# Kernel optimization log

Hardware: AMD Instinct MI355X
Metric: run time of the kernel (lower is better)

Reference implementation:

```python
import jax, jax.numpy as jnp
import numpy as np

N_NODES = 50000
N_EDGES = 800000
ND = 64
ED = 32
MSG = 128
HID = 256
N_AGENTS = 25000


def setup_inputs() -> dict:
    key = jax.random.key(0)
    ks = jax.random.split(key, 12)
    s = lambda k, shape, fan: jax.random.normal(k, shape, jnp.float32) / np.sqrt(fan)
    return {
        'node_feats': jax.random.normal(ks[0], (N_NODES, ND), jnp.float32),
        'edge_feats': jax.random.normal(ks[1], (N_EDGES, ED), jnp.float32),
        'W_msg1': s(ks[2], (2 * ND + ED, HID), 2 * ND + ED),
        'b_msg1': jnp.zeros((HID,), jnp.float32),
        'W_msg2': s(ks[3], (HID, MSG), HID),
        'b_msg2': jnp.zeros((MSG,), jnp.float32),
        'w_gate': s(ks[4], (MSG, 1), MSG),
        'b_gate': jnp.zeros((1,), jnp.float32),
        'W_h1': s(ks[5], (MSG, HID), MSG),
        'b_h1': jnp.zeros((HID,), jnp.float32),
        'W_h2': s(ks[6], (HID, HID), HID),
        'b_h2': jnp.zeros((HID,), jnp.float32),
        'W_out': s(ks[7], (HID, 1), HID),
        'b_out': jnp.zeros((1,), jnp.float32),
        'senders': jax.random.randint(ks[8], (N_EDGES,), 0, N_NODES, jnp.int32),
        'receivers': jax.random.randint(ks[9], (N_EDGES,), 0, N_NODES, jnp.int32),
        'n_agents': N_AGENTS,
    }


def reference(node_feats, edge_feats, W_msg1, b_msg1, W_msg2, b_msg2,
              w_gate, b_gate, W_h1, b_h1, W_h2, b_h2, W_out, b_out,
              senders, receivers, n_agents):
    n_nodes = node_feats.shape[0]
    # gather sender/receiver features, build edge messages (gather-transform)
    msg_in = jnp.concatenate(
        [node_feats[senders], node_feats[receivers], edge_feats], axis=-1)  # [E, 2*ND+ED]
    h = jax.nn.relu(msg_in @ W_msg1 + b_msg1)                               # [E, HID]
    msg = jax.nn.relu(h @ W_msg2 + b_msg2)                                  # [E, MSG]
    # per-receiver segment softmax attention
    logits = (msg @ w_gate + b_gate)[:, 0]                                  # [E]
    seg_max = jax.ops.segment_max(logits, receivers, num_segments=n_nodes)  # [N]
    e = jnp.exp(logits - seg_max[receivers])                                # [E]
    denom = jax.ops.segment_sum(e, receivers, num_segments=n_nodes)         # [N]
    attn = e / (denom[receivers] + 1e-9)                                    # [E]
    # scatter-aggregate messages to nodes
    aggr = jax.ops.segment_sum(attn[:, None] * msg, receivers,
                               num_segments=n_nodes)                        # [N, MSG]
    # node_type == 0: agent nodes are the first n_agents nodes
    x = aggr[:n_agents]                                                     # [A, MSG]
    # head MLP
    x = jax.nn.relu(x @ W_h1 + b_h1)
    x = jax.nn.relu(x @ W_h2 + b_h2)
    # Dense(1) + tanh
    return jnp.tanh(x @ W_out + b_out)                                      # [A, 1]
```

## Files before the change

### kernel.cpp

```cpp
#include <hip/hip_runtime.h>
#include <hip/hip_bf16.h>

#define N_NODES  50000
#define N_EDGES  800000
#define ND       64
#define ED       32
#define MSGD     128
#define HIDD     256
#define N_AGENTS 25000
#define EPAD     800064

typedef _Float16 f16;
typedef __attribute__((ext_vector_type(4))) _Float16 f16x4;
typedef __attribute__((ext_vector_type(8))) _Float16 f16x8;
typedef __attribute__((ext_vector_type(4))) float f32x4;
typedef unsigned short u16;
typedef unsigned int   u32;
typedef unsigned long long u64;

__global__ __launch_bounds__(256) void pack_weights(
    const float* __restrict__ W1, const float* __restrict__ W2,
    const float* __restrict__ Wh1, const float* __restrict__ Wh2,
    f16* __restrict__ F1, f16* __restrict__ F2,
    f16* __restrict__ F3, f16* __restrict__ F4)
{
    int tid  = blockIdx.x * 256 + threadIdx.x;
    int grp  = tid >> 6, lane = tid & 63;
    const float* W; f16* D; int NT, stride, gl;
    if      (grp < 80)  { W = W1;  D = F1; NT = 16; stride = 256; gl = grp; }
    else if (grp < 144) { W = W2;  D = F2; NT = 8;  stride = 128; gl = grp - 80; }
    else if (grp < 208) { W = Wh1; D = F3; NT = 16; stride = 256; gl = grp - 144; }
    else if (grp < 336) { W = Wh2; D = F4; NT = 16; stride = 256; gl = grp - 208; }
    else return;
    int ks = gl / NT, nt = gl - ks * NT;
    int n  = nt * 16 + (lane & 15);
    int k0 = ks * 32 + (lane >> 4) * 8;
    f16* dst = D + ((size_t)gl * 64 + lane) * 8;
    #pragma unroll
    for (int j = 0; j < 8; ++j)
        dst[j] = (f16)W[(size_t)(k0 + j) * stride + n];
}

__global__ __launch_bounds__(256) void compact_kernel(
    const int* __restrict__ recv, const float* __restrict__ nf,
    f16* __restrict__ nf16, int* __restrict__ rankb,
    int* __restrict__ deg)
{
    int i = blockIdx.x * 256 + threadIdx.x;
    {
        float4 v = ((const float4*)nf)[i];
        f16x4 h;
        h.x = (f16)v.x; h.y = (f16)v.y; h.z = (f16)v.z; h.w = (f16)v.w;
        ((f16x4*)nf16)[i] = h;
    }
    int r = recv[i];
    if (r < N_AGENTS)
        rankb[i] = atomicAdd(&deg[r], 1);
}

__global__ __launch_bounds__(1024) void prefix_kernel(
    const int* __restrict__ deg, int* __restrict__ off)
{
    __shared__ int part[1024];
    int t = threadIdx.x;
    int i0 = t * 25;
    int s = 0;
    #pragma unroll 1
    for (int i = 0; i < 25; ++i) {
        int idx = i0 + i;
        if (idx < N_AGENTS) s += deg[idx];
    }
    part[t] = s;
    __syncthreads();
    for (int d = 1; d < 1024; d <<= 1) {
        int v = (t >= d) ? part[t - d] : 0;
        __syncthreads();
        part[t] += v;
        __syncthreads();
    }
    int run = (t == 0) ? 0 : part[t - 1];
    #pragma unroll 1
    for (int i = 0; i < 25; ++i) {
        int idx = i0 + i;
        if (idx < N_AGENTS) {
            off[idx] = run;
            run += deg[idx];
        }
    }
    if (t == 1023) off[N_AGENTS] = part[1023];
}

__global__ __launch_bounds__(256) void scatter_kernel(
    const int* __restrict__ recv, const int* __restrict__ send,
    const int* __restrict__ rankb, const int* __restrict__ off,
    int* __restrict__ eidb, int* __restrict__ sendb, int* __restrict__ recvb)
{
    int i = blockIdx.x * 256 + threadIdx.x;
    int r = recv[i];
    if (r < N_AGENTS) {
        int pos = off[r] + rankb[i];
        eidb[pos]  = i;
        sendb[pos] = send[i];
        recvb[pos] = r;
    }
}

__global__ __launch_bounds__(512, 4) void edge_mlp_mfma(
    const f16* __restrict__ nf16, const float* __restrict__ ef,
    const f16* __restrict__ F1, const f16* __restrict__ F2,
    const float* __restrict__ b1, const float* __restrict__ b2,
    const float* __restrict__ wg, const float* __restrict__ bg,
    const int* __restrict__ sendb, const int* __restrict__ recvb,
    const int* __restrict__ eidb, const int* __restrict__ cnt,
    f16* __restrict__ msg_out, float* __restrict__ evals)
{
    __shared__ __align__(16) f16 XF[2][10][64][8];
    __shared__ __align__(16) f16 HB[16][64][8];
    __shared__ __align__(16) f16 msgt[32][136];
    __shared__ float lpart[8][32];

    const int tid  = threadIdx.x;
    const int wv   = tid >> 6;
    const int lane = tid & 63;
    const int q    = lane >> 4;
    const int li   = lane & 15;
    const int cntv   = cnt[0];
    const int ntiles = (cntv + 31) >> 5;

    const int xcd   = blockIdx.x & 7;
    const int bslot = blockIdx.x >> 3;
    const int tstep = gridDim.x >> 3;
    const int T8    = (ntiles + 7) >> 3;
    const int tend  = min((xcd + 1) * T8, ntiles);
    const int t0    = xcd * T8 + bslot;

    f16x8 w1[2][5], w2[8];
    #pragma unroll
    for (int ntl = 0; ntl < 2; ++ntl)
        #pragma unroll
        for (int ks = 0; ks < 5; ++ks)
            w1[ntl][ks] = *(const f16x8*)(F1 + (((size_t)(ks * 16 + 2 * wv + ntl)) * 64 + lane) * 8);
    #pragma unroll
    for (int ks = 0; ks < 8; ++ks)
        w2[ks] = *(const f16x8*)(F2 + (((size_t)(ks * 8 + wv)) * 64 + lane) * 8);

    const float4 ba  = *(const float4*)&b1[wv * 32 + q * 4];
    const float4 bb  = *(const float4*)&b1[wv * 32 + 16 + q * 4];
    const float4 bc  = *(const float4*)&b2[wv * 16 + q * 4];
    const float4 wg4 = *(const float4*)&wg[wv * 16 + q * 4];
    const float  bgv = bg[0];

    if (t0 < tend) {
        const int e0p = t0 * 32;
        f16 (*XFd)[64][8] = XF[0];
        for (int idx = tid; idx < 768; idx += 512) {
            int e = idx / 24, g = idx - e * 24;
            int cp = e0p + e;
            if (g < 16) {
                int node = (g < 8) ? sendb[cp] : recvb[cp];
                f16x8 h = *(const f16x8*)(nf16 + (size_t)node * 64 + (g & 7) * 8);
                int slt = (e >> 4) * 5 + (g >> 2);
                int ln  = (e & 15) + 16 * (g & 3);
                *(f16x8*)&XFd[slt][ln][0] = h;
            } else {
                int eid = eidb[cp];
                float4 v = ((const float4*)ef)[(size_t)eid * 8 + (g - 16)];
                int k0  = 128 + (g - 16) * 4;
                int slt = (e >> 4) * 5 + 4;
                int ln  = (e & 15) + 16 * ((k0 & 31) >> 3);
                int j0  = k0 & 7;
                f16x4 h;
                h.x = (f16)v.x; h.y = (f16)v.y; h.z = (f16)v.z; h.w = (f16)v.w;
                *(f16x4*)&XFd[slt][ln][j0] = h;
            }
        }
    }
    __syncthreads();

    int p = 0;
    for (int t = t0; t < tend; t += tstep) {
        const int e0 = t * 32;
        const int tn = t + tstep;

        if (tn < tend) {
            const int e0n = tn * 32;
            f16 (*XFd)[64][8] = XF[p ^ 1];
            for (int idx = tid; idx < 768; idx += 512) {
                int e = idx / 24, g = idx - e * 24;
                int cp = e0n + e;
                if (g < 16) {
                    int node = (g < 8) ? sendb[cp] : recvb[cp];
                    f16x8 h = *(const f16x8*)(nf16 + (size_t)node * 64 + (g & 7) * 8);
                    int slt = (e >> 4) * 5 + (g >> 2);
                    int ln  = (e & 15) + 16 * (g & 3);
                    *(f16x8*)&XFd[slt][ln][0] = h;
                } else {
                    int eid = eidb[cp];
                    float4 v = ((const float4*)ef)[(size_t)eid * 8 + (g - 16)];
                    int k0  = 128 + (g - 16) * 4;
                    int slt = (e >> 4) * 5 + 4;
                    int ln  = (e & 15) + 16 * ((k0 & 31) >> 3);
                    int j0  = k0 & 7;
                    f16x4 h;
                    h.x = (f16)v.x; h.y = (f16)v.y; h.z = (f16)v.z; h.w = (f16)v.w;
                    *(f16x4*)&XFd[slt][ln][j0] = h;
                }
            }
        }

        f32x4 acc[2][2];
        acc[0][0] = f32x4{ba.x, ba.y, ba.z, ba.w}; acc[1][0] = acc[0][0];
        acc[0][1] = f32x4{bb.x, bb.y, bb.z, bb.w}; acc[1][1] = acc[0][1];
        #pragma unroll
        for (int ks = 0; ks < 5; ++ks)
            #pragma unroll
            for (int eh = 0; eh < 2; ++eh) {
                f16x8 xh = *(const f16x8*)XF[p][eh * 5 + ks][lane];
                acc[eh][0] = __builtin_amdgcn_mfma_f32_16x16x32_f16(w1[0][ks], xh, acc[eh][0], 0, 0, 0);
                acc[eh][1] = __builtin_amdgcn_mfma_f32_16x16x32_f16(w1[1][ks], xh, acc[eh][1], 0, 0, 0);
            }
        #pragma unroll
        for (int eh = 0; eh < 2; ++eh)
            #pragma unroll
            for (int ntl = 0; ntl < 2; ++ntl) {
                f16x4 hv;
                hv.x = (f16)fmaxf(acc[eh][ntl][0], 0.f);
                hv.y = (f16)fmaxf(acc[eh][ntl][1], 0.f);
                hv.z = (f16)fmaxf(acc[eh][ntl][2], 0.f);
                hv.w = (f16)fmaxf(acc[eh][ntl][3], 0.f);
                int l2 = li + 16 * (2 * ntl + (q >> 1));
                int j0 = (q & 1) * 4;
                *(f16x4*)&HB[eh * 8 + wv][l2][j0] = hv;
            }
        __syncthreads();

        f32x4 acc2[2];
        acc2[0] = f32x4{bc.x, bc.y, bc.z, bc.w}; acc2[1] = acc2[0];
        #pragma unroll
        for (int ks2 = 0; ks2 < 8; ++ks2)
            #pragma unroll
            for (int eh = 0; eh < 2; ++eh) {
                f16x8 hh = *(const f16x8*)HB[eh * 8 + ks2][lane];
                acc2[eh] = __builtin_amdgcn_mfma_f32_16x16x32_f16(w2[ks2], hh, acc2[eh], 0, 0, 0);
            }
        {
            float pr[2];
            #pragma unroll
            for (int eh = 0; eh < 2; ++eh) {
                float v0 = fmaxf(acc2[eh][0], 0.f);
                float v1 = fmaxf(acc2[eh][1], 0.f);
                float v2 = fmaxf(acc2[eh][2], 0.f);
                float v3 = fmaxf(acc2[eh][3], 0.f);
                f16x4 mm;
                mm.x = (f16)v0; mm.y = (f16)v1; mm.z = (f16)v2; mm.w = (f16)v3;
                *(f16x4*)&msgt[eh * 16 + li][wv * 16 + q * 4] = mm;
                float pp = v0 * wg4.x + v1 * wg4.y + v2 * wg4.z + v3 * wg4.w;
                pp += __shfl_xor(pp, 16, 64);
                pp += __shfl_xor(pp, 32, 64);
                pr[eh] = pp;
            }
            if (lane < 16) {
                lpart[wv][li]      = pr[0];
                lpart[wv][16 + li] = pr[1];
            }
        }
        __syncthreads();

        {
            int row = tid >> 4, cg = tid & 15;
            *(uint4*)(msg_out + (size_t)(e0 + row) * 128 + cg * 8) =
                *(const uint4*)&msgt[row][cg * 8];
        }
        if (tid < 32) {
            float s2 = bgv;
            #pragma unroll
            for (int w = 0; w < 8; ++w) s2 += lpart[w][tid];
            evals[e0 + tid] = expf(s2);
        }
        p ^= 1;
    }
}

__global__ __launch_bounds__(1024, 4) void agg_agent_mfma(
    const int* __restrict__ off, const float* __restrict__ evals,
    const f16* __restrict__ msg,
    const f16* __restrict__ F3, const f16* __restrict__ F4,
    const float* __restrict__ bh1, const float* __restrict__ bh2,
    const float* __restrict__ Wout, const float* __restrict__ bout,
    float* __restrict__ out)
{
    __shared__ __align__(16) f16 XA[8][64][8];
    __shared__ __align__(16) f16 HB2[16][64][8];
    __shared__ float lpart[16][32];

    const int tid  = threadIdx.x;
    const int wv   = tid >> 6;
    const int lane = tid & 63;
    const int q    = lane >> 4;
    const int li   = lane & 15;
    const int a0i  = blockIdx.x * 32;

    {
        int g = tid >> 5, c = tid & 31;
        int r = a0i + g;
        float den = 1e-9f;
        float4 acc = make_float4(0.f, 0.f, 0.f, 0.f);
        if (r < N_AGENTS) {
            int beg = off[r], end = off[r + 1];
            const u64* mp = (const u64*)(msg + (size_t)beg * 128) + c;
            int pp = beg;
            for (; pp + 3 < end; pp += 4, mp += 128) {
                float e0 = evals[pp], e1 = evals[pp + 1];
                float e2 = evals[pp + 2], e3 = evals[pp + 3];
                u64 u0 = mp[0], u1 = mp[32], u2 = mp[64], u3 = mp[96];
                den += (e0 + e1) + (e2 + e3);
                union { u64 u; f16 h[4]; } c0, c1, c2, c3;
                c0.u = u0; c1.u = u1; c2.u = u2; c3.u = u3;
                acc.x = fmaf(e3, (float)c3.h[0], fmaf(e2, (float)c2.h[0],
                        fmaf(e1, (float)c1.h[0], fmaf(e0, (float)c0.h[0], acc.x))));
                acc.y = fmaf(e3, (float)c3.h[1], fmaf(e2, (float)c2.h[1],
                        fmaf(e1, (float)c1.h[1], fmaf(e0, (float)c0.h[1], acc.y))));
                acc.z = fmaf(e3, (float)c3.h[2], fmaf(e2, (float)c2.h[2],
                        fmaf(e1, (float)c1.h[2], fmaf(e0, (float)c0.h[2], acc.z))));
                acc.w = fmaf(e3, (float)c3.h[3], fmaf(e2, (float)c2.h[3],
                        fmaf(e1, (float)c1.h[3], fmaf(e0, (float)c0.h[3], acc.w))));
            }
            for (; pp < end; ++pp, mp += 32) {
                float e = evals[pp];
                den += e;
                union { u64 u; f16 h[4]; } cv; cv.u = *mp;
                acc.x = fmaf(e, (float)cv.h[0], acc.x);
                acc.y = fmaf(e, (float)cv.h[1], acc.y);
                acc.z = fmaf(e, (float)cv.h[2], acc.z);
                acc.w = fmaf(e, (float)cv.h[3], acc.w);
            }
        }
        float inv = 1.0f / den;
        int k0   = c * 4;
        int slot = (g >> 4) * 4 + (k0 >> 5);
        int ln   = (g & 15) + 16 * ((k0 & 31) >> 3);
        int j0   = k0 & 7;
        f16x4 h;
        h.x = (f16)(acc.x * inv); h.y = (f16)(acc.y * inv);
        h.z = (f16)(acc.z * inv); h.w = (f16)(acc.w * inv);
        *(f16x4*)&XA[slot][ln][j0] = h;
    }
    __syncthreads();

    f16x8 wh1[4], wh2[8];
    #pragma unroll
    for (int ks = 0; ks < 4; ++ks)
        wh1[ks] = *(const f16x8*)(F3 + (((size_t)(ks * 16 + wv)) * 64 + lane) * 8);
    #pragma unroll
    for (int ks = 0; ks < 8; ++ks)
        wh2[ks] = *(const f16x8*)(F4 + (((size_t)(ks * 16 + wv)) * 64 + lane) * 8);

    f32x4 acc[2] = {};
    #pragma unroll
    for (int ks = 0; ks < 4; ++ks)
        #pragma unroll
        for (int eh = 0; eh < 2; ++eh) {
            f16x8 xh = *(const f16x8*)XA[eh * 4 + ks][lane];
            acc[eh] = __builtin_amdgcn_mfma_f32_16x16x32_f16(wh1[ks], xh, acc[eh], 0, 0, 0);
        }
    {
        const float4 b1v = ((const float4*)bh1)[wv * 4 + q];
        #pragma unroll
        for (int eh = 0; eh < 2; ++eh) {
            f16x4 hv;
            hv.x = (f16)fmaxf(acc[eh][0] + b1v.x, 0.f);
            hv.y = (f16)fmaxf(acc[eh][1] + b1v.y, 0.f);
            hv.z = (f16)fmaxf(acc[eh][2] + b1v.z, 0.f);
            hv.w = (f16)fmaxf(acc[eh][3] + b1v.w, 0.f);
            int l2 = li + 16 * ((wv & 1) * 2 + (q >> 1));
            int j0 = (q & 1) * 4;
            *(f16x4*)&HB2[eh * 8 + (wv >> 1)][l2][j0] = hv;
        }
    }
    __syncthreads();

    f32x4 acc2[2] = {};
    #pragma unroll
    for (int ks2 = 0; ks2 < 8; ++ks2)
        #pragma unroll
        for (int eh = 0; eh < 2; ++eh) {
            f16x8 hh = *(const f16x8*)HB2[eh * 8 + ks2][lane];
            acc2[eh] = __builtin_amdgcn_mfma_f32_16x16x32_f16(wh2[ks2], hh, acc2[eh], 0, 0, 0);
        }
    {
        const float4 b2v = ((const float4*)bh2)[wv * 4 + q];
        const float4 wo4 = ((const float4*)Wout)[wv * 4 + q];
        float pr[2];
        #pragma unroll
        for (int eh = 0; eh < 2; ++eh) {
            float pp = fmaxf(acc2[eh][0] + b2v.x, 0.f) * wo4.x
                     + fmaxf(acc2[eh][1] + b2v.y, 0.f) * wo4.y
                     + fmaxf(acc2[eh][2] + b2v.z, 0.f) * wo4.z
                     + fmaxf(acc2[eh][3] + b2v.w, 0.f) * wo4.w;
            pp += __shfl_xor(pp, 16, 64);
            pp += __shfl_xor(pp, 32, 64);
            pr[eh] = pp;
        }
        if (lane < 16) {
            lpart[wv][li]      = pr[0];
            lpart[wv][16 + li] = pr[1];
        }
    }
    __syncthreads();

    if (tid < 32 && a0i + tid < N_AGENTS) {
        float s = bout[0];
        #pragma unroll
        for (int w = 0; w < 16; ++w) s += lpart[w][tid];
        out[a0i + tid] = tanhf(s);
    }
}

extern "C" void kernel_launch(void* const* d_in, const int* in_sizes, int n_in,
                              void* d_out, int out_size, void* d_ws, size_t ws_size,
                              hipStream_t stream)
{
    const float* nf   = (const float*)d_in[0];
    const float* ef   = (const float*)d_in[1];
    const float* W1   = (const float*)d_in[2];
    const float* b1   = (const float*)d_in[3];
    const float* W2   = (const float*)d_in[4];
    const float* b2   = (const float*)d_in[5];
    const float* wg   = (const float*)d_in[6];
    const float* bg   = (const float*)d_in[7];
    const float* Wh1  = (const float*)d_in[8];
    const float* bh1  = (const float*)d_in[9];
    const float* Wh2  = (const float*)d_in[10];
    const float* bh2  = (const float*)d_in[11];
    const float* Wout = (const float*)d_in[12];
    const float* bout = (const float*)d_in[13];
    const int*   send = (const int*)d_in[14];
    const int*   recv = (const int*)d_in[15];

    char* ws = (char*)d_ws;
    int* deg    = (int*)ws;            ws += (size_t)N_AGENTS * 4;
    int* eidb   = (int*)ws;            ws += (size_t)EPAD * 4;
    int* sendb  = (int*)ws;            ws += (size_t)EPAD * 4;
    int* recvb  = (int*)ws;            ws += (size_t)EPAD * 4;
    size_t zero_bytes = (size_t)(ws - (char*)d_ws);
    int* rankb  = (int*)ws;            ws += (size_t)N_EDGES * 4;
    int* off    = (int*)ws;            ws += (size_t)(N_AGENTS + 8) * 4;
    float* evals = (float*)ws;         ws += (size_t)EPAD * 4;
    f16* nf16   = (f16*)ws;            ws += (size_t)N_NODES * ND * 2;
    f16* F1     = (f16*)ws;            ws += (size_t)160 * 256 * 2;
    f16* F2     = (f16*)ws;            ws += (size_t)256 * 128 * 2;
    f16* F3     = (f16*)ws;            ws += (size_t)128 * 256 * 2;
    f16* F4     = (f16*)ws;            ws += (size_t)256 * 256 * 2;
    f16* msg    = (f16*)ws;

    hipMemsetAsync(d_ws, 0, zero_bytes, stream);

    pack_weights<<<84, 256, 0, stream>>>(W1, W2, Wh1, Wh2, F1, F2, F3, F4);
    compact_kernel<<<N_EDGES / 256, 256, 0, stream>>>(
        recv, nf, nf16, rankb, deg);
    prefix_kernel<<<1, 1024, 0, stream>>>(deg, off);
    scatter_kernel<<<N_EDGES / 256, 256, 0, stream>>>(
        recv, send, rankb, off, eidb, sendb, recvb);
    edge_mlp_mfma<<<512, 512, 0, stream>>>(
        nf16, ef, F1, F2, b1, b2, wg, bg, sendb, recvb, eidb, off + N_AGENTS, msg, evals);
    agg_agent_mfma<<<(N_AGENTS + 31) / 32, 1024, 0, stream>>>(
        off, evals, msg, F3, F4, bh1, bh2, Wout, bout, (float*)d_out);
}
```

Before: 415.8 us.

## Software-pipeline edge gathers across tiles and fuse weight packing into compact kernel

```diff
diff --git a/kernel.cpp b/kernel.cpp
--- a/kernel.cpp
+++ b/kernel.cpp
@@ -18,35 +18,41 @@
 typedef unsigned int   u32;
 typedef unsigned long long u64;
 
-__global__ __launch_bounds__(256) void pack_weights(
+#define WG_BARRIER() do {                                       \
+    __builtin_amdgcn_sched_barrier(0);                          \
+    asm volatile("s_waitcnt lgkmcnt(0)" ::: "memory");          \
+    __builtin_amdgcn_s_barrier();                               \
+    __builtin_amdgcn_sched_barrier(0);                          \
+} while (0)
+
+__global__ __launch_bounds__(256) void compact_pack_kernel(
+    const int* __restrict__ recv, const float* __restrict__ nf,
+    f16* __restrict__ nf16, int* __restrict__ rankb, int* __restrict__ deg,
     const float* __restrict__ W1, const float* __restrict__ W2,
     const float* __restrict__ Wh1, const float* __restrict__ Wh2,
     f16* __restrict__ F1, f16* __restrict__ F2,
     f16* __restrict__ F3, f16* __restrict__ F4)
 {
-    int tid  = blockIdx.x * 256 + threadIdx.x;
-    int grp  = tid >> 6, lane = tid & 63;
-    const float* W; f16* D; int NT, stride, gl;
-    if      (grp < 80)  { W = W1;  D = F1; NT = 16; stride = 256; gl = grp; }
-    else if (grp < 144) { W = W2;  D = F2; NT = 8;  stride = 128; gl = grp - 80; }
-    else if (grp < 208) { W = Wh1; D = F3; NT = 16; stride = 256; gl = grp - 144; }
-    else if (grp < 336) { W = Wh2; D = F4; NT = 16; stride = 256; gl = grp - 208; }
-    else return;
-    int ks = gl / NT, nt = gl - ks * NT;
-    int n  = nt * 16 + (lane & 15);
-    int k0 = ks * 32 + (lane >> 4) * 8;
-    f16* dst = D + ((size_t)gl * 64 + lane) * 8;
-    #pragma unroll
-    for (int j = 0; j < 8; ++j)
-        dst[j] = (f16)W[(size_t)(k0 + j) * stride + n];
-}
-
-__global__ __launch_bounds__(256) void compact_kernel(
-    const int* __restrict__ recv, const float* __restrict__ nf,
-    f16* __restrict__ nf16, int* __restrict__ rankb,
-    int* __restrict__ deg)
-{
-    int i = blockIdx.x * 256 + threadIdx.x;
+    int b = blockIdx.x;
+    if (b >= N_EDGES / 256) {
+        int tid  = (b - N_EDGES / 256) * 256 + threadIdx.x;
+        int grp  = tid >> 6, lane = tid & 63;
+        const float* W; f16* D; int NT, stride, gl;
+        if      (grp < 80)  { W = W1;  D = F1; NT = 16; stride = 256; gl = grp; }
+        else if (grp < 144) { W = W2;  D = F2; NT = 8;  stride = 128; gl = grp - 80; }
+        else if (grp < 208) { W = Wh1; D = F3; NT = 16; stride = 256; gl = grp - 144; }
+        else if (grp < 336) { W = Wh2; D = F4; NT = 16; stride = 256; gl = grp - 208; }
+        else return;
+        int ks = gl / NT, nt = gl - ks * NT;
+        int n  = nt * 16 + (lane & 15);
+        int k0 = ks * 32 + (lane >> 4) * 8;
+        f16* dst = D + ((size_t)gl * 64 + lane) * 8;
+        #pragma unroll
+        for (int j = 0; j < 8; ++j)
+            dst[j] = (f16)W[(size_t)(k0 + j) * stride + n];
+        return;
+    }
+    int i = b * 256 + threadIdx.x;
     {
         float4 v = ((const float4*)nf)[i];
         f16x4 h;
@@ -114,7 +120,7 @@
     const int* __restrict__ eidb, const int* __restrict__ cnt,
     f16* __restrict__ msg_out, float* __restrict__ evals)
 {
-    __shared__ __align__(16) f16 XF[2][10][64][8];
+    __shared__ __align__(16) f16 XF[2][5120];
     __shared__ __align__(16) f16 HB[16][64][8];
     __shared__ __align__(16) f16 msgt[32][136];
     __shared__ float lpart[8][32];
@@ -134,6 +140,36 @@
     const int tend  = min((xcd + 1) * T8, ntiles);
     const int t0    = xcd * T8 + bslot;
 
+    const int  e_0 = tid / 24,          g_0 = tid - (tid / 24) * 24;
+    const int  e_1 = (tid + 512) / 24,  g_1 = (tid + 512) - ((tid + 512) / 24) * 24;
+    const bool has1 = (tid < 256);
+    const int* ip0 = (g_0 < 8) ? sendb : (g_0 < 16 ? recvb : eidb);
+    const int* ip1 = (g_1 < 8) ? sendb : (g_1 < 16 ? recvb : eidb);
+    auto lds_off = [](int e, int g) -> int {
+        if (g < 16)
+            return (((e >> 4) * 5 + (g >> 2)) * 64 + (e & 15) + 16 * (g & 3)) * 8;
+        int k0 = 128 + (g - 16) * 4;
+        return (((e >> 4) * 5 + 4) * 64 + (e & 15) + 16 * ((k0 & 31) >> 3)) * 8 + (k0 & 7);
+    };
+    const int lo0 = lds_off(e_0, g_0);
+    const int lo1 = lds_off(e_1, g_1);
+    auto gslot = [&](int g, int i) -> uint4 {
+        return (g < 16)
+            ? *(const uint4*)(nf16 + (size_t)i * 64 + (g & 7) * 8)
+            : *(const uint4*)(ef + (size_t)i * 32 + (g - 16) * 4);
+    };
+    auto wslot = [&](f16* xb, int lo, int g, uint4 s) {
+        if (g < 16) {
+            *(uint4*)(xb + lo) = s;
+        } else {
+            union { uint4 u; float4 f; } cv; cv.u = s;
+            f16x4 h;
+            h.x = (f16)cv.f.x; h.y = (f16)cv.f.y;
+            h.z = (f16)cv.f.z; h.w = (f16)cv.f.w;
+            *(f16x4*)(xb + lo) = h;
+        }
+    };
+
     f16x8 w1[2][5], w2[8];
     #pragma unroll
     for (int ntl = 0; ntl < 2; ++ntl)
@@ -150,62 +186,36 @@
     const float4 wg4 = *(const float4*)&wg[wv * 16 + q * 4];
     const float  bgv = bg[0];
 
+    int i0 = 0, i1 = 0;
     if (t0 < tend) {
-        const int e0p = t0 * 32;
-        f16 (*XFd)[64][8] = XF[0];
-        for (int idx = tid; idx < 768; idx += 512) {
-            int e = idx / 24, g = idx - e * 24;
-            int cp = e0p + e;
-            if (g < 16) {
-                int node = (g < 8) ? sendb[cp] : recvb[cp];
-                f16x8 h = *(const f16x8*)(nf16 + (size_t)node * 64 + (g & 7) * 8);
-                int slt = (e >> 4) * 5 + (g >> 2);
-                int ln  = (e & 15) + 16 * (g & 3);
-                *(f16x8*)&XFd[slt][ln][0] = h;
-            } else {
-                int eid = eidb[cp];
-                float4 v = ((const float4*)ef)[(size_t)eid * 8 + (g - 16)];
-                int k0  = 128 + (g - 16) * 4;
-                int slt = (e >> 4) * 5 + 4;
-                int ln  = (e & 15) + 16 * ((k0 & 31) >> 3);
-                int j0  = k0 & 7;
-                f16x4 h;
-                h.x = (f16)v.x; h.y = (f16)v.y; h.z = (f16)v.z; h.w = (f16)v.w;
-                *(f16x4*)&XFd[slt][ln][j0] = h;
-            }
+        int j0i = ip0[t0 * 32 + e_0];
+        wslot(XF[0], lo0, g_0, gslot(g_0, j0i));
+        if (has1) {
+            int j1i = ip1[t0 * 32 + e_1];
+            wslot(XF[0], lo1, g_1, gslot(g_1, j1i));
+        }
+        if (t0 + tstep < tend) {
+            i0 = ip0[(t0 + tstep) * 32 + e_0];
+            if (has1) i1 = ip1[(t0 + tstep) * 32 + e_1];
         }
     }
     __syncthreads();
 
     int p = 0;
     for (int t = t0; t < tend; t += tstep) {
-        const int e0 = t * 32;
-        const int tn = t + tstep;
-
+        const int e0  = t * 32;
+        const int tn  = t + tstep;
+        const int tnn = tn + tstep;
+
+        uint4 s0{}, s1{};
         if (tn < tend) {
-            const int e0n = tn * 32;
-            f16 (*XFd)[64][8] = XF[p ^ 1];
-            for (int idx = tid; idx < 768; idx += 512) {
-                int e = idx / 24, g = idx - e * 24;
-                int cp = e0n + e;
-                if (g < 16) {
-                    int node = (g < 8) ? sendb[cp] : recvb[cp];
-                    f16x8 h = *(const f16x8*)(nf16 + (size_t)node * 64 + (g & 7) * 8);
-                    int slt = (e >> 4) * 5 + (g >> 2);
-                    int ln  = (e & 15) + 16 * (g & 3);
-                    *(f16x8*)&XFd[slt][ln][0] = h;
-                } else {
-                    int eid = eidb[cp];
-                    float4 v = ((const float4*)ef)[(size_t)eid * 8 + (g - 16)];
-                    int k0  = 128 + (g - 16) * 4;
-                    int slt = (e >> 4) * 5 + 4;
-                    int ln  = (e & 15) + 16 * ((k0 & 31) >> 3);
-                    int j0  = k0 & 7;
-                    f16x4 h;
-                    h.x = (f16)v.x; h.y = (f16)v.y; h.z = (f16)v.z; h.w = (f16)v.w;
-                    *(f16x4*)&XFd[slt][ln][j0] = h;
-                }
-            }
+            s0 = gslot(g_0, i0);
+            if (has1) s1 = gslot(g_1, i1);
+        }
+        int ni0 = 0, ni1 = 0;
+        if (tnn < tend) {
+            ni0 = ip0[tnn * 32 + e_0];
+            if (has1) ni1 = ip1[tnn * 32 + e_1];
         }
 
         f32x4 acc[2][2];
@@ -215,7 +225,7 @@
         for (int ks = 0; ks < 5; ++ks)
             #pragma unroll
             for (int eh = 0; eh < 2; ++eh) {
-                f16x8 xh = *(const f16x8*)XF[p][eh * 5 + ks][lane];
+                f16x8 xh = *(const f16x8*)&XF[p][((eh * 5 + ks) * 64 + lane) * 8];
                 acc[eh][0] = __builtin_amdgcn_mfma_f32_16x16x32_f16(w1[0][ks], xh, acc[eh][0], 0, 0, 0);
                 acc[eh][1] = __builtin_amdgcn_mfma_f32_16x16x32_f16(w1[1][ks], xh, acc[eh][1], 0, 0, 0);
             }
@@ -232,7 +242,7 @@
                 int j0 = (q & 1) * 4;
                 *(f16x4*)&HB[eh * 8 + wv][l2][j0] = hv;
             }
-        __syncthreads();
+        WG_BARRIER();
 
         f32x4 acc2[2];
         acc2[0] = f32x4{bc.x, bc.y, bc.z, bc.w}; acc2[1] = acc2[0];
@@ -264,7 +274,13 @@
                 lpart[wv][16 + li] = pr[1];
             }
         }
-        __syncthreads();
+        WG_BARRIER();
+
+        if (tn < tend) {
+            f16* xb = XF[p ^ 1];
+            wslot(xb, lo0, g_0, s0);
+            if (has1) wslot(xb, lo1, g_1, s1);
+        }
 
         {
             int row = tid >> 4, cg = tid & 15;
@@ -277,6 +293,9 @@
             for (int w = 0; w < 8; ++w) s2 += lpart[w][tid];
             evals[e0 + tid] = expf(s2);
         }
+
+        i0 = ni0; i1 = ni1;
+        WG_BARRIER();
         p ^= 1;
     }
 }
@@ -455,9 +474,8 @@
 
     hipMemsetAsync(d_ws, 0, zero_bytes, stream);
 
-    pack_weights<<<84, 256, 0, stream>>>(W1, W2, Wh1, Wh2, F1, F2, F3, F4);
-    compact_kernel<<<N_EDGES / 256, 256, 0, stream>>>(
-        recv, nf, nf16, rankb, deg);
+    compact_pack_kernel<<<N_EDGES / 256 + 84, 256, 0, stream>>>(
+        recv, nf, nf16, rankb, deg, W1, W2, Wh1, Wh2, F1, F2, F3, F4);
     prefix_kernel<<<1, 1024, 0, stream>>>(deg, off);
     scatter_kernel<<<N_EDGES / 256, 256, 0, stream>>>(
         recv, send, rankb, off, eidb, sendb, recvb);
```

New measurement: 424.5 us. 1.02x slower.

## Fuse softmax-weighted aggregation into edge MLP via atomics, merge weight packing

Applied to the files above, without the earlier changes.

```diff
diff --git a/kernel.cpp b/kernel.cpp
--- a/kernel.cpp
+++ b/kernel.cpp
@@ -18,35 +18,34 @@
 typedef unsigned int   u32;
 typedef unsigned long long u64;
 
-__global__ __launch_bounds__(256) void pack_weights(
+__global__ __launch_bounds__(256) void compact_pack_kernel(
+    const int* __restrict__ recv, const float* __restrict__ nf,
+    f16* __restrict__ nf16, int* __restrict__ rankb, int* __restrict__ deg,
     const float* __restrict__ W1, const float* __restrict__ W2,
     const float* __restrict__ Wh1, const float* __restrict__ Wh2,
     f16* __restrict__ F1, f16* __restrict__ F2,
     f16* __restrict__ F3, f16* __restrict__ F4)
 {
-    int tid  = blockIdx.x * 256 + threadIdx.x;
-    int grp  = tid >> 6, lane = tid & 63;
-    const float* W; f16* D; int NT, stride, gl;
-    if      (grp < 80)  { W = W1;  D = F1; NT = 16; stride = 256; gl = grp; }
-    else if (grp < 144) { W = W2;  D = F2; NT = 8;  stride = 128; gl = grp - 80; }
-    else if (grp < 208) { W = Wh1; D = F3; NT = 16; stride = 256; gl = grp - 144; }
-    else if (grp < 336) { W = Wh2; D = F4; NT = 16; stride = 256; gl = grp - 208; }
-    else return;
-    int ks = gl / NT, nt = gl - ks * NT;
-    int n  = nt * 16 + (lane & 15);
-    int k0 = ks * 32 + (lane >> 4) * 8;
-    f16* dst = D + ((size_t)gl * 64 + lane) * 8;
-    #pragma unroll
-    for (int j = 0; j < 8; ++j)
-        dst[j] = (f16)W[(size_t)(k0 + j) * stride + n];
-}
-
-__global__ __launch_bounds__(256) void compact_kernel(
-    const int* __restrict__ recv, const float* __restrict__ nf,
-    f16* __restrict__ nf16, int* __restrict__ rankb,
-    int* __restrict__ deg)
-{
-    int i = blockIdx.x * 256 + threadIdx.x;
+    int b = blockIdx.x;
+    if (b >= N_EDGES / 256) {
+        int tid  = (b - N_EDGES / 256) * 256 + threadIdx.x;
+        int grp  = tid >> 6, lane = tid & 63;
+        const float* W; f16* D; int NT, stride, gl;
+        if      (grp < 80)  { W = W1;  D = F1; NT = 16; stride = 256; gl = grp; }
+        else if (grp < 144) { W = W2;  D = F2; NT = 8;  stride = 128; gl = grp - 80; }
+        else if (grp < 208) { W = Wh1; D = F3; NT = 16; stride = 256; gl = grp - 144; }
+        else if (grp < 336) { W = Wh2; D = F4; NT = 16; stride = 256; gl = grp - 208; }
+        else return;
+        int ks = gl / NT, nt = gl - ks * NT;
+        int n  = nt * 16 + (lane & 15);
+        int k0 = ks * 32 + (lane >> 4) * 8;
+        f16* dst = D + ((size_t)gl * 64 + lane) * 8;
+        #pragma unroll
+        for (int j = 0; j < 8; ++j)
+            dst[j] = (f16)W[(size_t)(k0 + j) * stride + n];
+        return;
+    }
+    int i = b * 256 + threadIdx.x;
     {
         float4 v = ((const float4*)nf)[i];
         f16x4 h;
@@ -112,12 +111,14 @@
     const float* __restrict__ wg, const float* __restrict__ bg,
     const int* __restrict__ sendb, const int* __restrict__ recvb,
     const int* __restrict__ eidb, const int* __restrict__ cnt,
-    f16* __restrict__ msg_out, float* __restrict__ evals)
+    float* __restrict__ aggr, float* __restrict__ den)
 {
     __shared__ __align__(16) f16 XF[2][10][64][8];
     __shared__ __align__(16) f16 HB[16][64][8];
     __shared__ __align__(16) f16 msgt[32][136];
-    __shared__ float lpart[8][32];
+    __shared__ float lpart[8][64];
+    __shared__ float evt[64];
+    __shared__ int   recvt[64];
 
     const int tid  = threadIdx.x;
     const int wv   = tid >> 6;
@@ -133,6 +134,8 @@
     const int T8    = (ntiles + 7) >> 3;
     const int tend  = min((xcd + 1) * T8, ntiles);
     const int t0    = xcd * T8 + bslot;
+
+    if (tid < 256) lpart[tid >> 5][32 + (tid & 31)] = 0.f;
 
     f16x8 w1[2][5], w2[8];
     #pragma unroll
@@ -266,24 +269,53 @@
         }
         __syncthreads();
 
+        if (tid < 64) {
+            int r = -1;
+            int pos = e0 + tid;
+            if (tid < 32 && pos < cntv) r = recvt[0] = 0, r = recvb[pos];
+            float s2 = bgv;
+            #pragma unroll
+            for (int w = 0; w < 8; ++w) s2 += lpart[w][tid];
+            float e = expf(s2);
+            if (r < 0) e = 0.f;
+            evt[tid]   = e;
+            recvt[tid] = r;
+            float a = e;
+            #pragma unroll
+            for (int k = 1; k <= 16; k <<= 1) {
+                int   rn = __shfl_down(r, k, 64);
+                float an = __shfl_down(a, k, 64);
+                if (tid + k < 64 && rn == r) a += an;
+            }
+            int rp = __shfl_up(r, 1, 64);
+            if ((tid == 0 || r != rp) && r >= 0)
+                atomicAdd(&den[r], a);
+        }
+        __syncthreads();
+
         {
-            int row = tid >> 4, cg = tid & 15;
-            *(uint4*)(msg_out + (size_t)(e0 + row) * 128 + cg * 8) =
-                *(const uint4*)&msgt[row][cg * 8];
-        }
-        if (tid < 32) {
-            float s2 = bgv;
-            #pragma unroll
-            for (int w = 0; w < 8; ++w) s2 += lpart[w][tid];
-            evals[e0 + tid] = expf(s2);
+            int col = tid >> 2, seg = tid & 3;
+            float run = 0.f; int rprev = -1;
+            #pragma unroll
+            for (int j = 0; j < 8; ++j) {
+                int row = seg * 8 + j;
+                int r = recvt[row];
+                if (r != rprev) {
+                    if (rprev >= 0)
+                        atomicAdd(&aggr[(size_t)rprev * 128 + col], run);
+                    run = 0.f; rprev = r;
+                }
+                run += evt[row] * (float)msgt[row][col];
+            }
+            if (rprev >= 0)
+                atomicAdd(&aggr[(size_t)rprev * 128 + col], run);
         }
         p ^= 1;
     }
 }
 
 __global__ __launch_bounds__(1024, 4) void agg_agent_mfma(
-    const int* __restrict__ off, const float* __restrict__ evals,
-    const f16* __restrict__ msg,
+    const float* __restrict__ aggr, const float* __restrict__ den,
     const f16* __restrict__ F3, const f16* __restrict__ F4,
     const float* __restrict__ bh1, const float* __restrict__ bh2,
     const float* __restrict__ Wout, const float* __restrict__ bout,
@@ -303,46 +335,20 @@
     {
         int g = tid >> 5, c = tid & 31;
         int r = a0i + g;
-        float den = 1e-9f;
-        float4 acc = make_float4(0.f, 0.f, 0.f, 0.f);
+        float4 a = make_float4(0.f, 0.f, 0.f, 0.f);
+        float d = 1e-9f;
         if (r < N_AGENTS) {
-            int beg = off[r], end = off[r + 1];
-            const u64* mp = (const u64*)(msg + (size_t)beg * 128) + c;
-            int pp = beg;
-            for (; pp + 3 < end; pp += 4, mp += 128) {
-                float e0 = evals[pp], e1 = evals[pp + 1];
-                float e2 = evals[pp + 2], e3 = evals[pp + 3];
-                u64 u0 = mp[0], u1 = mp[32], u2 = mp[64], u3 = mp[96];
-                den += (e0 + e1) + (e2 + e3);
-                union { u64 u; f16 h[4]; } c0, c1, c2, c3;
-                c0.u = u0; c1.u = u1; c2.u = u2; c3.u = u3;
-                acc.x = fmaf(e3, (float)c3.h[0], fmaf(e2, (float)c2.h[0],
-                        fmaf(e1, (float)c1.h[0], fmaf(e0, (float)c0.h[0], acc.x))));
-                acc.y = fmaf(e3, (float)c3.h[1], fmaf(e2, (float)c2.h[1],
-                        fmaf(e1, (float)c1.h[1], fmaf(e0, (float)c0.h[1], acc.y))));
-                acc.z = fmaf(e3, (float)c3.h[2], fmaf(e2, (float)c2.h[2],
-                        fmaf(e1, (float)c1.h[2], fmaf(e0, (float)c0.h[2], acc.z))));
-                acc.w = fmaf(e3, (float)c3.h[3], fmaf(e2, (float)c2.h[3],
-                        fmaf(e1, (float)c1.h[3], fmaf(e0, (float)c0.h[3], acc.w))));
-            }
-            for (; pp < end; ++pp, mp += 32) {
-                float e = evals[pp];
-                den += e;
-                union { u64 u; f16 h[4]; } cv; cv.u = *mp;
-                acc.x = fmaf(e, (float)cv.h[0], acc.x);
-                acc.y = fmaf(e, (float)cv.h[1], acc.y);
-                acc.z = fmaf(e, (float)cv.h[2], acc.z);
-                acc.w = fmaf(e, (float)cv.h[3], acc.w);
-            }
-        }
-        float inv = 1.0f / den;
+            a = *(const float4*)&aggr[(size_t)r * 128 + c * 4];
+            d += den[r];
+        }
+        float inv = 1.0f / d;
         int k0   = c * 4;
         int slot = (g >> 4) * 4 + (k0 >> 5);
         int ln   = (g & 15) + 16 * ((k0 & 31) >> 3);
         int j0   = k0 & 7;
         f16x4 h;
-        h.x = (f16)(acc.x * inv); h.y = (f16)(acc.y * inv);
-        h.z = (f16)(acc.z * inv); h.w = (f16)(acc.w * inv);
+        h.x = (f16)(a.x * inv); h.y = (f16)(a.y * inv);
+        h.z = (f16)(a.z * inv); h.w = (f16)(a.w * inv);
         *(f16x4*)&XA[slot][ln][j0] = h;
     }
     __syncthreads();
@@ -442,27 +448,27 @@
     int* eidb   = (int*)ws;            ws += (size_t)EPAD * 4;
     int* sendb  = (int*)ws;            ws += (size_t)EPAD * 4;
     int* recvb  = (int*)ws;            ws += (size_t)EPAD * 4;
+    float* den  = (float*)ws;          ws += (size_t)N_AGENTS * 4;
+    float* aggr = (float*)ws;          ws += (size_t)N_AGENTS * 128 * 4;
     size_t zero_bytes = (size_t)(ws - (char*)d_ws);
     int* rankb  = (int*)ws;            ws += (size_t)N_EDGES * 4;
     int* off    = (int*)ws;            ws += (size_t)(N_AGENTS + 8) * 4;
-    float* evals = (float*)ws;         ws += (size_t)EPAD * 4;
     f16* nf16   = (f16*)ws;            ws += (size_t)N_NODES * ND * 2;
     f16* F1     = (f16*)ws;            ws += (size_t)160 * 256 * 2;
     f16* F2     = (f16*)ws;            ws += (size_t)256 * 128 * 2;
     f16* F3     = (f16*)ws;            ws += (size_t)128 * 256 * 2;
     f16* F4     = (f16*)ws;            ws += (size_t)256 * 256 * 2;
-    f16* msg    = (f16*)ws;
 
     hipMemsetAsync(d_ws, 0, zero_bytes, stream);
 
-    pack_weights<<<84, 256, 0, stream>>>(W1, W2, Wh1, Wh2, F1, F2, F3, F4);
-    compact_kernel<<<N_EDGES / 256, 256, 0, stream>>>(
-        recv, nf, nf16, rankb, deg);
+    compact_pack_kernel<<<N_EDGES / 256 + 84, 256, 0, stream>>>(
+        recv, nf, nf16, rankb, deg, W1, W2, Wh1, Wh2, F1, F2, F3, F4);
     prefix_kernel<<<1, 1024, 0, stream>>>(deg, off);
     scatter_kernel<<<N_EDGES / 256, 256, 0, stream>>>(
         recv, send, rankb, off, eidb, sendb, recvb);
     edge_mlp_mfma<<<512, 512, 0, stream>>>(
-        nf16, ef, F1, F2, b1, b2, wg, bg, sendb, recvb, eidb, off + N_AGENTS, msg, evals);
+        nf16, ef, F1, F2, b1, b2, wg, bg, sendb, recvb, eidb, off + N_AGENTS,
+        aggr, den);
     agg_agent_mfma<<<(N_AGENTS + 31) / 32, 1024, 0, stream>>>(
-        off, evals, msg, F3, F4, bh1, bh2, Wout, bout, (float*)d_out);
-}
+        aggr, den, F3, F4, bh1, bh2, Wout, bout, (float*)d_out);
+}
```

Result: slower. 522.6 us (+25.7%).

## Merge weight packing into compaction, parallelize prefix scan, pack edge indices

Applied to the files above, without the earlier changes.

```diff
diff --git a/kernel.cpp b/kernel.cpp
--- a/kernel.cpp
+++ b/kernel.cpp
@@ -18,35 +18,34 @@
 typedef unsigned int   u32;
 typedef unsigned long long u64;
 
-__global__ __launch_bounds__(256) void pack_weights(
+__global__ __launch_bounds__(256) void compact_pack_kernel(
+    const int* __restrict__ recv, const float* __restrict__ nf,
+    f16* __restrict__ nf16, int* __restrict__ rankb, int* __restrict__ deg,
     const float* __restrict__ W1, const float* __restrict__ W2,
     const float* __restrict__ Wh1, const float* __restrict__ Wh2,
     f16* __restrict__ F1, f16* __restrict__ F2,
     f16* __restrict__ F3, f16* __restrict__ F4)
 {
-    int tid  = blockIdx.x * 256 + threadIdx.x;
-    int grp  = tid >> 6, lane = tid & 63;
-    const float* W; f16* D; int NT, stride, gl;
-    if      (grp < 80)  { W = W1;  D = F1; NT = 16; stride = 256; gl = grp; }
-    else if (grp < 144) { W = W2;  D = F2; NT = 8;  stride = 128; gl = grp - 80; }
-    else if (grp < 208) { W = Wh1; D = F3; NT = 16; stride = 256; gl = grp - 144; }
-    else if (grp < 336) { W = Wh2; D = F4; NT = 16; stride = 256; gl = grp - 208; }
-    else return;
-    int ks = gl / NT, nt = gl - ks * NT;
-    int n  = nt * 16 + (lane & 15);
-    int k0 = ks * 32 + (lane >> 4) * 8;
-    f16* dst = D + ((size_t)gl * 64 + lane) * 8;
-    #pragma unroll
-    for (int j = 0; j < 8; ++j)
-        dst[j] = (f16)W[(size_t)(k0 + j) * stride + n];
-}
-
-__global__ __launch_bounds__(256) void compact_kernel(
-    const int* __restrict__ recv, const float* __restrict__ nf,
-    f16* __restrict__ nf16, int* __restrict__ rankb,
-    int* __restrict__ deg)
-{
-    int i = blockIdx.x * 256 + threadIdx.x;
+    int b = blockIdx.x;
+    if (b >= N_EDGES / 256) {
+        int tid  = (b - N_EDGES / 256) * 256 + threadIdx.x;
+        int grp  = tid >> 6, lane = tid & 63;
+        const float* W; f16* D; int NT, stride, gl;
+        if      (grp < 80)  { W = W1;  D = F1; NT = 16; stride = 256; gl = grp; }
+        else if (grp < 144) { W = W2;  D = F2; NT = 8;  stride = 128; gl = grp - 80; }
+        else if (grp < 208) { W = Wh1; D = F3; NT = 16; stride = 256; gl = grp - 144; }
+        else if (grp < 336) { W = Wh2; D = F4; NT = 16; stride = 256; gl = grp - 208; }
+        else return;
+        int ks = gl / NT, nt = gl - ks * NT;
+        int n  = nt * 16 + (lane & 15);
+        int k0 = ks * 32 + (lane >> 4) * 8;
+        f16* dst = D + ((size_t)gl * 64 + lane) * 8;
+        #pragma unroll
+        for (int j = 0; j < 8; ++j)
+            dst[j] = (f16)W[(size_t)(k0 + j) * stride + n];
+        return;
+    }
+    int i = b * 256 + threadIdx.x;
     {
         float4 v = ((const float4*)nf)[i];
         f16x4 h;
@@ -58,50 +57,61 @@
         rankb[i] = atomicAdd(&deg[r], 1);
 }
 
-__global__ __launch_bounds__(1024) void prefix_kernel(
-    const int* __restrict__ deg, int* __restrict__ off)
+__global__ __launch_bounds__(1024) void prefix_part(
+    const int* __restrict__ deg, int* __restrict__ bsum)
+{
+    __shared__ int red[16];
+    int b = blockIdx.x, t = threadIdx.x;
+    int v = (t < 1000) ? deg[b * 1000 + t] : 0;
+    #pragma unroll
+    for (int k = 1; k <= 32; k <<= 1) v += __shfl_xor(v, k, 64);
+    if ((t & 63) == 0) red[t >> 6] = v;
+    __syncthreads();
+    if (t == 0) {
+        int s = 0;
+        #pragma unroll
+        for (int w = 0; w < 16; ++w) s += red[w];
+        bsum[b] = s;
+    }
+}
+
+__global__ __launch_bounds__(1024) void prefix_scan(
+    const int* __restrict__ deg, const int* __restrict__ bsum,
+    int* __restrict__ off)
 {
     __shared__ int part[1024];
-    int t = threadIdx.x;
-    int i0 = t * 25;
-    int s = 0;
-    #pragma unroll 1
-    for (int i = 0; i < 25; ++i) {
-        int idx = i0 + i;
-        if (idx < N_AGENTS) s += deg[idx];
-    }
-    part[t] = s;
+    __shared__ int basesh;
+    int b = blockIdx.x, t = threadIdx.x;
+    if (t == 0) {
+        int s = 0;
+        for (int j = 0; j < b; ++j) s += bsum[j];
+        basesh = s;
+    }
+    int v = (t < 1000) ? deg[b * 1000 + t] : 0;
+    part[t] = v;
     __syncthreads();
     for (int d = 1; d < 1024; d <<= 1) {
-        int v = (t >= d) ? part[t - d] : 0;
+        int u = (t >= d) ? part[t - d] : 0;
         __syncthreads();
-        part[t] += v;
+        part[t] += u;
         __syncthreads();
     }
-    int run = (t == 0) ? 0 : part[t - 1];
-    #pragma unroll 1
-    for (int i = 0; i < 25; ++i) {
-        int idx = i0 + i;
-        if (idx < N_AGENTS) {
-            off[idx] = run;
-            run += deg[idx];
-        }
-    }
-    if (t == 1023) off[N_AGENTS] = part[1023];
+    int incl = part[t];
+    int base = basesh;
+    if (t < 1000) off[b * 1000 + t] = base + incl - v;
+    if (b == 24 && t == 999) off[N_AGENTS] = base + incl;
 }
 
 __global__ __launch_bounds__(256) void scatter_kernel(
     const int* __restrict__ recv, const int* __restrict__ send,
     const int* __restrict__ rankb, const int* __restrict__ off,
-    int* __restrict__ eidb, int* __restrict__ sendb, int* __restrict__ recvb)
+    int4* __restrict__ idx4)
 {
     int i = blockIdx.x * 256 + threadIdx.x;
     int r = recv[i];
     if (r < N_AGENTS) {
         int pos = off[r] + rankb[i];
-        eidb[pos]  = i;
-        sendb[pos] = send[i];
-        recvb[pos] = r;
+        idx4[pos] = make_int4(i, send[i], r, 0);
     }
 }
 
@@ -110,8 +120,7 @@
     const f16* __restrict__ F1, const f16* __restrict__ F2,
     const float* __restrict__ b1, const float* __restrict__ b2,
     const float* __restrict__ wg, const float* __restrict__ bg,
-    const int* __restrict__ sendb, const int* __restrict__ recvb,
-    const int* __restrict__ eidb, const int* __restrict__ cnt,
+    const int* __restrict__ idx4i, const int* __restrict__ cnt,
     f16* __restrict__ msg_out, float* __restrict__ evals)
 {
     __shared__ __align__(16) f16 XF[2][10][64][8];
@@ -157,13 +166,13 @@
             int e = idx / 24, g = idx - e * 24;
             int cp = e0p + e;
             if (g < 16) {
-                int node = (g < 8) ? sendb[cp] : recvb[cp];
+                int node = idx4i[cp * 4 + ((g < 8) ? 1 : 2)];
                 f16x8 h = *(const f16x8*)(nf16 + (size_t)node * 64 + (g & 7) * 8);
                 int slt = (e >> 4) * 5 + (g >> 2);
                 int ln  = (e & 15) + 16 * (g & 3);
                 *(f16x8*)&XFd[slt][ln][0] = h;
             } else {
-                int eid = eidb[cp];
+                int eid = idx4i[cp * 4];
                 float4 v = ((const float4*)ef)[(size_t)eid * 8 + (g - 16)];
                 int k0  = 128 + (g - 16) * 4;
                 int slt = (e >> 4) * 5 + 4;
@@ -189,13 +198,13 @@
                 int e = idx / 24, g = idx - e * 24;
                 int cp = e0n + e;
                 if (g < 16) {
-                    int node = (g < 8) ? sendb[cp] : recvb[cp];
+                    int node = idx4i[cp * 4 + ((g < 8) ? 1 : 2)];
                     f16x8 h = *(const f16x8*)(nf16 + (size_t)node * 64 + (g & 7) * 8);
                     int slt = (e >> 4) * 5 + (g >> 2);
                     int ln  = (e & 15) + 16 * (g & 3);
                     *(f16x8*)&XFd[slt][ln][0] = h;
                 } else {
-                    int eid = eidb[cp];
+                    int eid = idx4i[cp * 4];
                     float4 v = ((const float4*)ef)[(size_t)eid * 8 + (g - 16)];
                     int k0  = 128 + (g - 16) * 4;
                     int slt = (e >> 4) * 5 + 4;
@@ -438,12 +447,11 @@
     const int*   recv = (const int*)d_in[15];
 
     char* ws = (char*)d_ws;
-    int* deg    = (int*)ws;            ws += (size_t)N_AGENTS * 4;
-    int* eidb   = (int*)ws;            ws += (size_t)EPAD * 4;
-    int* sendb  = (int*)ws;            ws += (size_t)EPAD * 4;
-    int* recvb  = (int*)ws;            ws += (size_t)EPAD * 4;
+    int*  deg   = (int*)ws;            ws += (size_t)N_AGENTS * 4;
+    int4* idx4  = (int4*)ws;           ws += (size_t)EPAD * 16;
     size_t zero_bytes = (size_t)(ws - (char*)d_ws);
     int* rankb  = (int*)ws;            ws += (size_t)N_EDGES * 4;
+    int* bsum   = (int*)ws;            ws += 32 * 4;
     int* off    = (int*)ws;            ws += (size_t)(N_AGENTS + 8) * 4;
     float* evals = (float*)ws;         ws += (size_t)EPAD * 4;
     f16* nf16   = (f16*)ws;            ws += (size_t)N_NODES * ND * 2;
@@ -455,14 +463,15 @@
 
     hipMemsetAsync(d_ws, 0, zero_bytes, stream);
 
-    pack_weights<<<84, 256, 0, stream>>>(W1, W2, Wh1, Wh2, F1, F2, F3, F4);
-    compact_kernel<<<N_EDGES / 256, 256, 0, stream>>>(
-        recv, nf, nf16, rankb, deg);
-    prefix_kernel<<<1, 1024, 0, stream>>>(deg, off);
+    compact_pack_kernel<<<N_EDGES / 256 + 84, 256, 0, stream>>>(
+        recv, nf, nf16, rankb, deg, W1, W2, Wh1, Wh2, F1, F2, F3, F4);
+    prefix_part<<<25, 1024, 0, stream>>>(deg, bsum);
+    prefix_scan<<<25, 1024, 0, stream>>>(deg, bsum, off);
     scatter_kernel<<<N_EDGES / 256, 256, 0, stream>>>(
-        recv, send, rankb, off, eidb, sendb, recvb);
+        recv, send, rankb, off, idx4);
     edge_mlp_mfma<<<512, 512, 0, stream>>>(
-        nf16, ef, F1, F2, b1, b2, wg, bg, sendb, recvb, eidb, off + N_AGENTS, msg, evals);
+        nf16, ef, F1, F2, b1, b2, wg, bg, (const int*)idx4, off + N_AGENTS,
+        msg, evals);
     agg_agent_mfma<<<(N_AGENTS + 31) / 32, 1024, 0, stream>>>(
         off, evals, msg, F3, F4, bh1, bh2, Wout, bout, (float*)d_out);
 }
```

Result: faster. 364.6 us (-12.3%).
